# Optimization experiments

Measured on AMD Instinct MI355X. Metric: run time of the kernel, lower is better.

The kernel has to match this reference:

```python
import jax, jax.numpy as jnp
import numpy as np

L, B, Q, M, D, H, DH, DI = 4, 2, 1024, 1024, 1024, 16, 64, 4096


def setup_inputs() -> dict:
    key = jax.random.key(0)
    ks = jax.random.split(key, 10)
    s = 0.02
    return {
        "x": jax.random.normal(ks[0], (B, Q, D), jnp.float32),
        "memory": jax.random.normal(ks[1], (L, B, M, D), jnp.float32),
        "W_qkv": jax.random.normal(ks[2], (L, D, 3 * H * DH), jnp.float32) * s,
        "W_r": jax.random.normal(ks[3], (D, H * DH), jnp.float32) * s,
        "W_o": jax.random.normal(ks[4], (L, H * DH, D), jnp.float32) * s,
        "r_w_bias": jax.random.normal(ks[5], (H, DH), jnp.float32) * s,
        "r_r_bias": jax.random.normal(ks[6], (H, DH), jnp.float32) * s,
        "ln1_g": jnp.ones((L, D), jnp.float32),
        "ln1_b": jnp.zeros((L, D), jnp.float32),
        "ln2_g": jnp.ones((L, D), jnp.float32),
        "ln2_b": jnp.zeros((L, D), jnp.float32),
        "W_ff1": jax.random.normal(ks[7], (L, D, DI), jnp.float32) * s,
        "b_ff1": jnp.zeros((L, DI), jnp.float32),
        "W_ff2": jax.random.normal(ks[8], (L, DI, D), jnp.float32) * s,
        "b_ff2": jnp.zeros((L, D), jnp.float32),
    }


def _layernorm(x, g, b, eps=1e-5):
    mu = x.mean(-1, keepdims=True)
    var = ((x - mu) ** 2).mean(-1, keepdims=True)
    return (x - mu) * jax.lax.rsqrt(var + eps) * g + b


def _rel_shift(x):
    # Transformer-XL relative shift trick; x: [B, H, Q, K]
    b, h, q, k = x.shape
    x = jnp.pad(x, ((0, 0), (0, 0), (0, 0), (1, 0)))
    return x.reshape(b, h, k + 1, q)[:, :, 1:, :].reshape(b, h, q, k)


def reference(x, memory, W_qkv, W_r, W_o, r_w_bias, r_r_bias,
              ln1_g, ln1_b, ln2_g, ln2_b, W_ff1, b_ff1, W_ff2, b_ff2):
    Bsz, qlen, d = x.shape
    mlen = memory.shape[2]
    klen = mlen + qlen
    # sinusoidal relative position embedding for positions klen-1 .. 0
    pos = jnp.arange(klen - 1, -1, -1, dtype=x.dtype)
    inv_freq = 1.0 / (10000.0 ** (jnp.arange(0, d, 2, dtype=x.dtype) / d))
    sinusoid = pos[:, None] * inv_freq[None, :]
    p = jnp.concatenate([jnp.sin(sinusoid), jnp.cos(sinusoid)], axis=-1)  # [K, D]
    # causal mask with memory: query i may attend key j iff j <= i + mlen
    qi = jnp.arange(qlen)[:, None]
    kj = jnp.arange(klen)[None, :]
    blocked = kj > (qi + mlen)  # [Q, K]
    scale = 1.0 / np.sqrt(DH).astype(np.float32)
    for l in range(L):
        x_mem = jnp.concatenate([memory[l], x], axis=1)  # [B, K, D]
        heads = x_mem @ W_qkv[l]  # [B, K, 3*H*DH]
        qh, kh, vh = jnp.split(heads, 3, axis=-1)
        qh = qh[:, mlen:].reshape(Bsz, qlen, H, DH)
        kh = kh.reshape(Bsz, klen, H, DH)
        vh = vh.reshape(Bsz, klen, H, DH)
        r = (p @ W_r).reshape(klen, H, DH)  # [K, H, DH]
        AC = jnp.einsum('bqhd,bkhd->bhqk', qh + r_w_bias, kh)
        BD = _rel_shift(jnp.einsum('bqhd,khd->bhqk', qh + r_r_bias, r))
        score = (AC + BD) * scale
        score = jnp.where(blocked[None, None], -1e30, score)
        attn = jax.nn.softmax(score, axis=-1)
        out = jnp.einsum('bhqk,bkhd->bqhd', attn, vh).reshape(Bsz, qlen, H * DH) @ W_o[l]
        x = _layernorm(x + out, ln1_g[l], ln1_b[l])
        ff = jax.nn.relu(x @ W_ff1[l] + b_ff1[l]) @ W_ff2[l] + b_ff2[l]
        x = _layernorm(x + ff, ln2_g[l], ln2_b[l])
    return x
```

## Files before the change

kernel.cpp:

```cpp
#include <hip/hip_runtime.h>
#include <math.h>

#define L_  4
#define B_  2
#define Q_  1024
#define M_  1024
#define D_  1024
#define H_  16
#define DH_ 64
#define DI_ 4096
#define KL_ (M_ + Q_)

typedef __attribute__((ext_vector_type(8))) short short8v;
typedef __attribute__((ext_vector_type(4))) float f32x4;

__device__ __forceinline__ short f2bf(float f) {
    union { float f; unsigned u; } x; x.f = f;
    return (short)((x.u + 0x7FFFu + ((x.u >> 16) & 1)) >> 16);
}
__device__ __forceinline__ unsigned pack2bf(float a, float b) {
    return (unsigned)(unsigned short)f2bf(a) | ((unsigned)(unsigned short)f2bf(b) << 16);
}
__device__ __forceinline__ float bf2f(unsigned short u) {
    union { unsigned u; float f; } x; x.u = (unsigned)u << 16; return x.f;
}
__device__ __forceinline__ unsigned cvtpk(float lo, float hi) {
    unsigned r;
    asm("v_cvt_pk_bf16_f32 %0, %1, %2" : "=v"(r) : "v"(lo), "v"(hi));
    return r;
}
__device__ __forceinline__ void gload_lds16(const short* g, short* l) {
    __builtin_amdgcn_global_load_lds((const __attribute__((address_space(1))) unsigned int*)(const void*)g,
                                     (__attribute__((address_space(3))) unsigned int*)(void*)l, 16, 0, 0);
}
__device__ __forceinline__ int swz(int row) {
    return ((row & 7) ^ ((row >> 3) & 7)) << 3;
}

__global__ __launch_bounds__(256) void pos_emb_bf(short* __restrict__ p) {
    int idx = blockIdx.x * 256 + threadIdx.x;
    int k = idx >> 10;
    int i = idx & (D_ - 1);
    float pos = (float)(KL_ - 1 - k);
    int j = (i < D_ / 2) ? i : (i - D_ / 2);
    float invf = powf(10000.0f, -((float)(2 * j) / (float)D_));
    float ang = pos * invf;
    p[idx] = f2bf((i < D_ / 2) ? sinf(ang) : cosf(ang));
}

__global__ __launch_bounds__(256) void concat_bf(short* __restrict__ xmemb,
                                                 const float* __restrict__ mem_l,
                                                 const float* __restrict__ xc) {
    int idx = blockIdx.x * 256 + threadIdx.x;
    int d = idx & (D_ - 1);
    int k = (idx >> 10) & (KL_ - 1);
    int b = idx >> 21;
    float v = (k < M_) ? mem_l[((size_t)(b * M_ + k)) * D_ + d]
                       : xc[((size_t)(b * Q_ + (k - M_))) * D_ + d];
    xmemb[idx] = f2bf(v);
}

__global__ __launch_bounds__(256) void transp_bf(const float* __restrict__ in,
                                                 short* __restrict__ out,
                                                 int K, int N) {
    __shared__ float t[32][33];
    int r = threadIdx.x >> 3, c4 = (threadIdx.x & 7) * 4;
    float4 v = *(const float4*)(in + (size_t)(blockIdx.y * 32 + r) * N + blockIdx.x * 32 + c4);
    t[r][c4 + 0] = v.x; t[r][c4 + 1] = v.y; t[r][c4 + 2] = v.z; t[r][c4 + 3] = v.w;
    __syncthreads();
    uint2 o;
    o.x = pack2bf(t[c4 + 0][r], t[c4 + 1][r]);
    o.y = pack2bf(t[c4 + 2][r], t[c4 + 3][r]);
    *(uint2*)(out + (size_t)(blockIdx.x * 32 + r) * K + blockIdx.y * 32 + c4) = o;
}

template <int BIAS, int RELU, int OMODE, int TN, int KS = 1>
__global__ __launch_bounds__(256, 2) void gemm_bf(const short* __restrict__ A,
                                                  const short* __restrict__ BT,
                                                  const float* __restrict__ bias,
                                                  float* __restrict__ Cf,
                                                  short* __restrict__ C0,
                                                  short* __restrict__ C1,
                                                  short* __restrict__ C2,
                                                  int M, int N, int K) {
    __shared__ short A_s[128 * 32];
    __shared__ short B_s[TN * 32];
    const int tid = threadIdx.x;
    const int lane = tid & 63, w = tid >> 6;
    const int l15 = lane & 15, l4 = lane >> 4;
    constexpr int MF = (TN == 128) ? 4 : 2;
    const int wr = (TN == 128) ? (w >> 1) : w;
    const int wc = (TN == 128) ? (w & 1) : 0;
    const int arow0 = 32 * ((TN == 128) ? 2 * wr : w);
    const int brow0 = (TN == 128) ? 64 * wc : 0;
    const int row0 = blockIdx.y * 128, col0 = blockIdx.x * TN;
    const int kz = (KS == 2) ? blockIdx.z : 0;
    const int Kh = (KS == 2) ? (K >> 1) : K;
    const int kb = kz * Kh;

    const int lrow = lane >> 2;
    const int lk = (lane & 3) * 8;
    const short* Ag = A + (size_t)(row0 + 32 * w) * K;
    const short* Bg = BT + (size_t)(col0 + ((TN == 128) ? 32 : 16) * w) * K;

    f32x4 acc[MF][4] = {};

    for (int k0 = kb; k0 < kb + Kh; k0 += 32) {
        __syncthreads();
        gload_lds16(Ag + (size_t)lrow * K + k0 + lk,        &A_s[(32 * w) * 32]);
        gload_lds16(Ag + (size_t)(16 + lrow) * K + k0 + lk, &A_s[(32 * w + 16) * 32]);
        if (TN == 128) {
            gload_lds16(Bg + (size_t)lrow * K + k0 + lk,        &B_s[(32 * w) * 32]);
            gload_lds16(Bg + (size_t)(16 + lrow) * K + k0 + lk, &B_s[(32 * w + 16) * 32]);
        } else {
            gload_lds16(Bg + (size_t)lrow * K + k0 + lk,        &B_s[(16 * w) * 32]);
        }
        __syncthreads();
        short8v a[MF], bfr[4];
#pragma unroll
        for (int m = 0; m < MF; m++) a[m] = *(const short8v*)&A_s[(arow0 + 16 * m + l15) * 32 + 8 * l4];
#pragma unroll
        for (int n = 0; n < 4; n++) bfr[n] = *(const short8v*)&B_s[(brow0 + 16 * n + l15) * 32 + 8 * l4];
#pragma unroll
        for (int m = 0; m < MF; m++)
#pragma unroll
            for (int n = 0; n < 4; n++)
                acc[m][n] = __builtin_amdgcn_mfma_f32_16x16x32_bf16(a[m], bfr[n], acc[m][n], 0, 0, 0);
    }

    float* Cfz = Cf + (size_t)kz * M * N;
#pragma unroll
    for (int n = 0; n < 4; n++) {
        int col = col0 + brow0 + 16 * n + l15;
        float bv = (BIAS && (KS == 1 || kz == 0)) ? bias[col] : 0.0f;
#pragma unroll
        for (int m = 0; m < MF; m++) {
#pragma unroll
            for (int r = 0; r < 4; r++) {
                int row = row0 + arow0 + 16 * m + 4 * l4 + r;
                float v = acc[m][n][r] + bv;
                if (RELU) v = fmaxf(v, 0.0f);
                if (OMODE == 0) {
                    Cfz[(size_t)row * N + col] = v;
                } else if (OMODE == 1) {
                    C0[(size_t)row * N + col] = f2bf(v);
                } else {
                    int part = col >> 10, cc = col & 1023;
                    short* dst = part == 0 ? C0 : (part == 1 ? C1 : C2);
                    dst[(size_t)row * 1024 + cc] = f2bf(v);
                }
            }
        }
    }
}

__global__ __launch_bounds__(256, 2) void attn_mfma(const short* __restrict__ qbf,
                                                    const short* __restrict__ kbf,
                                                    const short* __restrict__ vbf,
                                                    const short* __restrict__ rbh,
                                                    const float* __restrict__ rwb,
                                                    const float* __restrict__ rrb,
                                                    short* __restrict__ attnob) {
    __shared__ short K_s[2][64 * 64];
    __shared__ short V_T[2][64 * 64];
    __shared__ short R_s[256 * 64];
    __shared__ short P_s[4][16 * 64];

    const int tid = threadIdx.x;
    const int lane = tid & 63, w = tid >> 6;
    const int l15 = lane & 15, l4 = lane >> 4;
    const int lr8 = lane >> 3, oct = lane & 7;
    const int d0 = (tid & 7) * 8;

    const int wg = blockIdx.x;
    const int xcd = wg & 7;
    const int qp = (wg >> 3) & 15;
    const int bl = (wg >> 7) & 3;
    const int h = xcd * 2 + (bl & 1);
    const int b = bl >> 1;
    const int qi = (qp & 1) ? (15 - (qp >> 1)) : (qp >> 1);
    const int q0 = qi * 64;
    const int nt = qi + 17;
    const int jbase0 = (Q_ - 64) - q0;

    size_t qrow = ((size_t)(b * KL_ + M_ + q0 + 16 * w + l15)) * 1024 + h * 64;
    union U8 { uint4 u; unsigned short us[8]; };
    U8 qa, qb2;
    qa.u  = *(const uint4*)(qbf + qrow + 8 * l4);
    qb2.u = *(const uint4*)(qbf + qrow + 32 + 8 * l4);
    short8v qwf0, qwf1, qrf0, qrf1;
#pragma unroll
    for (int i = 0; i < 8; i++) {
        float qv0 = bf2f(qa.us[i]), qv1 = bf2f(qb2.us[i]);
        int c0 = h * 64 + 8 * l4 + i, c1 = c0 + 32;
        qwf0[i] = f2bf(qv0 + rwb[c0]); qwf1[i] = f2bf(qv1 + rwb[c1]);
        qrf0[i] = f2bf(qv0 + rrb[c0]); qrf1[i] = f2bf(qv1 + rrb[c1]);
    }

#pragma unroll
    for (int c = 0; c < 2; c++) {
        int R0 = 16 * w + 8 * c;
        int row = R0 + lr8;
        gload_lds16(kbf + ((size_t)(b * KL_) + row) * 1024 + h * 64 + ((oct * 8) ^ swz(row)),
                    &K_s[0][R0 * 64]);
        gload_lds16(kbf + ((size_t)(b * KL_) + 64 + row) * 1024 + h * 64 + ((oct * 8) ^ swz(row)),
                    &K_s[1][R0 * 64]);
    }
#pragma unroll
    for (int c = 0; c < 8; c++) {
        int R0 = 64 * w + 8 * c;
        int row = R0 + lr8;
        int jl = jbase0 + row;
        gload_lds16(rbh + (size_t)jl * 1024 + h * 64 + ((oct * 8) ^ swz(row)),
                    &R_s[R0 * 64]);
    }
    {
        U8 cv0[2];
#pragma unroll
        for (int it = 0; it < 2; it++) {
            int rr = (tid + it * 256) >> 3;
            cv0[it].u = *(const uint4*)(vbf + ((size_t)(b * KL_) + rr) * 1024 + h * 64 + d0);
        }
#pragma unroll
        for (int it = 0; it < 2; it++) {
            int rr = (tid + it * 256) >> 3;
#pragma unroll
            for (int i = 0; i < 8; i++)
                V_T[0][(d0 + i) * 64 + (rr ^ swz(d0 + i))] = (short)cv0[it].us[i];
        }
    }
    asm volatile("s_waitcnt vmcnt(0) lgkmcnt(0)" ::: "memory");
    __builtin_amdgcn_sched_barrier(0);
    __builtin_amdgcn_s_barrier();
    __builtin_amdgcn_sched_barrier(0);

    f32x4 o[4];
    float m_r[4], l_p[4];
#pragma unroll
    for (int j = 0; j < 4; j++) o[j] = (f32x4){0.f, 0.f, 0.f, 0.f};
#pragma unroll
    for (int r = 0; r < 4; r++) { m_r[r] = -1e30f; l_p[r] = 0.0f; }

    int sl[4];
#pragma unroll
    for (int r = 0; r < 4; r++)
        sl[r] = (lane & 48) | ((l15 + 15 - (4 * l4 + r)) & 15);

    short* P_w = &P_s[w][0];
    const int rbase = 16 * (3 - w);

    f32x4 acA[4], zfA[5], acB[4], zfB[5];
#pragma unroll
    for (int j = 0; j < 4; j++) {
        int kk = 16 * j + l15, sz = swz(kk);
        short8v b0 = *(const short8v*)&K_s[0][kk * 64 + ((8 * l4) ^ sz)];
        short8v b1 = *(const short8v*)&K_s[0][kk * 64 + ((32 + 8 * l4) ^ sz)];
        f32x4 z = {0.f, 0.f, 0.f, 0.f};
        z = __builtin_amdgcn_mfma_f32_16x16x32_bf16(qwf0, b0, z, 0, 0, 0);
        z = __builtin_amdgcn_mfma_f32_16x16x32_bf16(qwf1, b1, z, 0, 0, 0);
        acA[j] = z;
    }
#pragma unroll
    for (int jb = 0; jb < 5; jb++) {
        int rp = (rbase + 16 * jb + l15) & 255;
        int sz = swz(rp);
        short8v b0 = *(const short8v*)&R_s[rp * 64 + ((8 * l4) ^ sz)];
        short8v b1 = *(const short8v*)&R_s[rp * 64 + ((32 + 8 * l4) ^ sz)];
        f32x4 z = {0.f, 0.f, 0.f, 0.f};
        z = __builtin_amdgcn_mfma_f32_16x16x32_bf16(qrf0, b0, z, 0, 0, 0);
        z = __builtin_amdgcn_mfma_f32_16x16x32_bf16(qrf1, b1, z, 0, 0, 0);
        zfA[jb] = z;
    }

    auto body = [&](f32x4 (&ac)[4], f32x4 (&zf)[5], f32x4 (&acn)[4], f32x4 (&zfn)[5], int t)
        __attribute__((always_inline)) {
        const int cb = t & 1, nb = (t + 1) & 1;
        uint4 pv2[2];
        if (t + 1 < nt) {
#pragma unroll
            for (int it = 0; it < 2; it++) {
                int rr = (tid + it * 256) >> 3;
                pv2[it] = *(const uint4*)(vbf + ((size_t)(b * KL_) + 64 * (t + 1) + rr) * 1024 + h * 64 + d0);
            }
        }
        if (t + 2 < nt) {
#pragma unroll
            for (int c = 0; c < 2; c++) {
                int R0 = 16 * w + 8 * c;
                int row = R0 + lr8;
                gload_lds16(kbf + ((size_t)(b * KL_) + 64 * (t + 2) + row) * 1024 + h * 64 + ((oct * 8) ^ swz(row)),
                            &K_s[cb][R0 * 64]);
            }
#pragma unroll
            for (int c = 0; c < 2; c++) {
                int R0 = 16 * w + 8 * c;
                int l0 = 64 * t + 256 + R0 + lr8;
                int ph = l0 & 255;
                int jl = jbase0 + l0;
                if (jl > KL_ - 1) jl = KL_ - 1;
                gload_lds16(rbh + (size_t)jl * 1024 + h * 64 + ((oct * 8) ^ swz(ph)),
                            &R_s[((64 * t + 256 + R0) & 255) * 64]);
            }
        }
        __builtin_amdgcn_sched_barrier(0);

        if (t + 1 < nt) {
            __builtin_amdgcn_s_setprio(1);
#pragma unroll
            for (int j = 0; j < 4; j++) {
                int kk = 16 * j + l15, sz = swz(kk);
                short8v b0 = *(const short8v*)&K_s[nb][kk * 64 + ((8 * l4) ^ sz)];
                short8v b1 = *(const short8v*)&K_s[nb][kk * 64 + ((32 + 8 * l4) ^ sz)];
                f32x4 z = {0.f, 0.f, 0.f, 0.f};
                z = __builtin_amdgcn_mfma_f32_16x16x32_bf16(qwf0, b0, z, 0, 0, 0);
                z = __builtin_amdgcn_mfma_f32_16x16x32_bf16(qwf1, b1, z, 0, 0, 0);
                acn[j] = z;
            }
#pragma unroll
            for (int jb = 0; jb < 5; jb++) {
                int rp = (64 * (t + 1) + rbase + 16 * jb + l15) & 255;
                int sz = swz(rp);
                short8v b0 = *(const short8v*)&R_s[rp * 64 + ((8 * l4) ^ sz)];
                short8v b1 = *(const short8v*)&R_s[rp * 64 + ((32 + 8 * l4) ^ sz)];
                f32x4 z = {0.f, 0.f, 0.f, 0.f};
                z = __builtin_amdgcn_mfma_f32_16x16x32_bf16(qrf0, b0, z, 0, 0, 0);
                z = __builtin_amdgcn_mfma_f32_16x16x32_bf16(qrf1, b1, z, 0, 0, 0);
                zfn[jb] = z;
            }
            __builtin_amdgcn_s_setprio(0);
        }

        float sv[4][4], lmax[4];
#pragma unroll
        for (int r = 0; r < 4; r++) {
            int row = 4 * l4 + r;
            float bq[5];
#pragma unroll
            for (int s = 0; s < 5; s++) bq[s] = __shfl(zf[s][r], sl[r]);
#pragma unroll
            for (int j = 0; j < 4; j++) {
                float bd = (l15 > row) ? bq[j + 1] : bq[j];
                sv[j][r] = (ac[j][r] + bd) * 0.125f;
            }
        }
        if (t == nt - 1) {
#pragma unroll
            for (int j = 0; j < 4; j++)
#pragma unroll
                for (int r = 0; r < 4; r++)
                    if (64 * t + 16 * j + l15 > q0 + 16 * w + 4 * l4 + r + M_) sv[j][r] = -1e30f;
        }
#pragma unroll
        for (int r = 0; r < 4; r++) lmax[r] = fmaxf(fmaxf(sv[0][r], sv[1][r]), fmaxf(sv[2][r], sv[3][r]));
        bool ok = true;
#pragma unroll
        for (int r = 0; r < 4; r++) ok = ok && (lmax[r] <= m_r[r] + 8.0f);
        if (!__all(ok)) {
#pragma unroll
            for (int r = 0; r < 4; r++) {
                float v = lmax[r];
                v = fmaxf(v, __shfl_xor(v, 1));
                v = fmaxf(v, __shfl_xor(v, 2));
                v = fmaxf(v, __shfl_xor(v, 4));
                v = fmaxf(v, __shfl_xor(v, 8));
                float mnew = fmaxf(m_r[r], v);
                float c = __expf(m_r[r] - mnew);
                m_r[r] = mnew;
                l_p[r] *= c;
#pragma unroll
                for (int jd = 0; jd < 4; jd++) o[jd][r] *= c;
            }
        }
#pragma unroll
        for (int j = 0; j < 4; j++)
#pragma unroll
            for (int r = 0; r < 4; r++) {
                float pp = __expf(sv[j][r] - m_r[r]);
                sv[j][r] = pp;
                l_p[r] += pp;
            }

#pragma unroll
        for (int r = 0; r < 4; r++) {
            int row = 4 * l4 + r;
            int sz = swz(row);
#pragma unroll
            for (int j = 0; j < 4; j += 2) {
                unsigned pk = cvtpk(sv[j][r], sv[j + 1][r]);
                P_w[row * 64 + ((16 * j + l15) ^ sz)] = (short)(pk & 0xffffu);
                P_w[row * 64 + ((16 * (j + 1) + l15) ^ sz)] = (short)(pk >> 16);
            }
        }
        int szp = swz(l15);
        short8v pa0 = *(const short8v*)&P_w[l15 * 64 + ((8 * l4) ^ szp)];
        short8v pa1 = *(const short8v*)&P_w[l15 * 64 + ((32 + 8 * l4) ^ szp)];
        __builtin_amdgcn_s_setprio(1);
#pragma unroll
        for (int jd = 0; jd < 4; jd++) {
            int dd = 16 * jd + l15, sz = swz(dd);
            short8v v0 = *(const short8v*)&V_T[cb][dd * 64 + ((8 * l4) ^ sz)];
            short8v v1 = *(const short8v*)&V_T[cb][dd * 64 + ((32 + 8 * l4) ^ sz)];
            o[jd] = __builtin_amdgcn_mfma_f32_16x16x32_bf16(pa0, v0, o[jd], 0, 0, 0);
            o[jd] = __builtin_amdgcn_mfma_f32_16x16x32_bf16(pa1, v1, o[jd], 0, 0, 0);
        }
        __builtin_amdgcn_s_setprio(0);

        if (t + 1 < nt) {
#pragma unroll
            for (int it = 0; it < 2; it++) {
                int rr = (tid + it * 256) >> 3;
                U8 cv; cv.u = pv2[it];
#pragma unroll
                for (int i = 0; i < 8; i++)
                    V_T[nb][(d0 + i) * 64 + (rr ^ swz(d0 + i))] = (short)cv.us[i];
            }
            asm volatile("s_waitcnt vmcnt(0) lgkmcnt(0)" ::: "memory");
            __builtin_amdgcn_sched_barrier(0);
            __builtin_amdgcn_s_barrier();
            __builtin_amdgcn_sched_barrier(0);
        }
    };

    int t = 0;
    while (t < nt) {
        body(acA, zfA, acB, zfB, t); t++;
        if (t >= nt) break;
        body(acB, zfB, acA, zfA, t); t++;
    }

    float l_r[4];
#pragma unroll
    for (int r = 0; r < 4; r++) {
        float v = l_p[r];
        v += __shfl_xor(v, 1);
        v += __shfl_xor(v, 2);
        v += __shfl_xor(v, 4);
        v += __shfl_xor(v, 8);
        l_r[r] = v;
    }
#pragma unroll
    for (int jd = 0; jd < 4; jd++) {
#pragma unroll
        for (int r = 0; r < 4; r++) {
            int qg = q0 + 16 * w + 4 * l4 + r;
            int dv = 16 * jd + l15;
            attnob[((size_t)(b * Q_ + qg)) * (H_ * DH_) + h * 64 + dv] = f2bf(o[jd][r] / l_r[r]);
        }
    }
}

__global__ __launch_bounds__(256) void ln_kernel(float* __restrict__ x,
                                                 short* __restrict__ xb,
                                                 const float* __restrict__ a1,
                                                 const float* __restrict__ a2,
                                                 const float* __restrict__ g,
                                                 const float* __restrict__ bb) {
    __shared__ float red[8];
    int row = blockIdx.x;
    int tid = threadIdx.x;
    float4 xv = ((const float4*)(x + (size_t)row * D_))[tid];
    float4 v1 = ((const float4*)(a1 + (size_t)row * D_))[tid];
    float4 v2 = ((const float4*)(a2 + (size_t)row * D_))[tid];
    float4 v;
    v.x = xv.x + v1.x + v2.x; v.y = xv.y + v1.y + v2.y;
    v.z = xv.z + v1.z + v2.z; v.w = xv.w + v1.w + v2.w;
    float s = v.x + v.y + v.z + v.w;
#pragma unroll
    for (int off = 32; off; off >>= 1) s += __shfl_xor(s, off);
    if ((tid & 63) == 0) red[tid >> 6] = s;
    __syncthreads();
    float mu = (red[0] + red[1] + red[2] + red[3]) * (1.0f / D_);
    float e0 = v.x - mu, e1 = v.y - mu, e2 = v.z - mu, e3 = v.w - mu;
    float sq = e0 * e0 + e1 * e1 + e2 * e2 + e3 * e3;
#pragma unroll
    for (int off = 32; off; off >>= 1) sq += __shfl_xor(sq, off);
    if ((tid & 63) == 0) red[4 + (tid >> 6)] = sq;
    __syncthreads();
    float var = (red[4] + red[5] + red[6] + red[7]) * (1.0f / D_);
    float rs = rsqrtf(var + 1e-5f);
    float4 gv = ((const float4*)g)[tid];
    float4 bv = ((const float4*)bb)[tid];
    float4 ov;
    ov.x = e0 * rs * gv.x + bv.x; ov.y = e1 * rs * gv.y + bv.y;
    ov.z = e2 * rs * gv.z + bv.z; ov.w = e3 * rs * gv.w + bv.w;
    ((float4*)(x + (size_t)row * D_))[tid] = ov;
    uint2 ob;
    ob.x = pack2bf(ov.x, ov.y);
    ob.y = pack2bf(ov.z, ov.w);
    *(uint2*)(xb + (size_t)row * D_ + tid * 4) = ob;
}

extern "C" void kernel_launch(void* const* d_in, const int* in_sizes, int n_in,
                              void* d_out, int out_size, void* d_ws, size_t ws_size,
                              hipStream_t stream) {
    const float* x    = (const float*)d_in[0];
    const float* mem  = (const float*)d_in[1];
    const float* Wqkv = (const float*)d_in[2];
    const float* Wr   = (const float*)d_in[3];
    const float* Wo   = (const float*)d_in[4];
    const float* rwb  = (const float*)d_in[5];
    const float* rrb  = (const float*)d_in[6];
    const float* ln1g = (const float*)d_in[7];
    const float* ln1b = (const float*)d_in[8];
    const float* ln2g = (const float*)d_in[9];
    const float* ln2b = (const float*)d_in[10];
    const float* Wff1 = (const float*)d_in[11];
    const float* bff1 = (const float*)d_in[12];
    const float* Wff2 = (const float*)d_in[13];
    const float* bff2 = (const float*)d_in[14];

    float* xc = (float*)d_out;

    short* WqkvT = (short*)d_ws;
    short* WoT   = WqkvT + 3145728;
    short* Wff1T = WoT + 1048576;
    short* Wff2T = Wff1T + 4194304;
    short* WrT   = Wff2T + 4194304;
    short* rbh   = WrT + 1048576;
    short* xmemb = rbh + 2097152;
    short* qbf   = xmemb + 4194304;
    short* kbf   = qbf + 4194304;
    short* vbf   = kbf + 4194304;
    short* attnob= vbf + 4194304;
    short* xcb   = attnob + 2097152;
    short* ff1ob = xcb + 2097152;
    float* addbuf= (float*)(ff1ob + 8388608);
    short* pbf   = ff1ob;

    transp_bf<<<dim3(32, 32), 256, 0, stream>>>(Wr, WrT, 1024, 1024);
    pos_emb_bf<<<(KL_ * D_) / 256, 256, 0, stream>>>(pbf);
    gemm_bf<0, 0, 1, 64><<<dim3(16, 16), 256, 0, stream>>>(
        pbf, WrT, nullptr, nullptr, rbh, nullptr, nullptr, KL_, 1024, 1024);

    hipMemcpyAsync(xc, x, (size_t)B_ * Q_ * D_ * sizeof(float),
                   hipMemcpyDeviceToDevice, stream);

    for (int l = 0; l < L_; l++) {
        const float* mem_l = mem + (size_t)l * B_ * M_ * D_;

        transp_bf<<<dim3(96, 32), 256, 0, stream>>>(Wqkv + (size_t)l * 3145728, WqkvT, 1024, 3072);
        transp_bf<<<dim3(32, 32), 256, 0, stream>>>(Wo + (size_t)l * 1048576, WoT, 1024, 1024);
        transp_bf<<<dim3(128, 32), 256, 0, stream>>>(Wff1 + (size_t)l * 4194304, Wff1T, 1024, 4096);
        transp_bf<<<dim3(32, 128), 256, 0, stream>>>(Wff2 + (size_t)l * 4194304, Wff2T, 4096, 1024);

        concat_bf<<<(B_ * KL_ * D_) / 256, 256, 0, stream>>>(xmemb, mem_l, xc);

        gemm_bf<0, 0, 2, 128><<<dim3(24, 32), 256, 0, stream>>>(
            xmemb, WqkvT, nullptr, nullptr, qbf, kbf, vbf, B_ * KL_, 3072, 1024);

        attn_mfma<<<B_ * H_ * (Q_ / 64), 256, 0, stream>>>(
            qbf, kbf, vbf, rbh, rwb, rrb, attnob);

        gemm_bf<0, 0, 0, 64, 2><<<dim3(16, 16, 2), 256, 0, stream>>>(
            attnob, WoT, nullptr, addbuf, nullptr, nullptr, nullptr, B_ * Q_, 1024, 1024);

        ln_kernel<<<B_ * Q_, 256, 0, stream>>>(xc, xcb, addbuf, addbuf + 2097152,
                                               ln1g + l * D_, ln1b + l * D_);

        gemm_bf<1, 1, 1, 128><<<dim3(32, 16), 256, 0, stream>>>(
            xcb, Wff1T, bff1 + (size_t)l * DI_, nullptr, ff1ob, nullptr, nullptr, B_ * Q_, 4096, 1024);

        gemm_bf<1, 0, 0, 64, 2><<<dim3(16, 16, 2), 256, 0, stream>>>(
            ff1ob, Wff2T, bff2 + (size_t)l * D_, addbuf, nullptr, nullptr, nullptr, B_ * Q_, 1024, 4096);

        ln_kernel<<<B_ * Q_, 256, 0, stream>>>(xc, xcb, addbuf, addbuf + 2097152,
                                               ln2g + l * D_, ln2b + l * D_);
    }
}
```

Measured before the change: 993.0 us.

## Compute Q only for current tokens and vectorize P stores via K-permuted V layout

Measured after the change: 1.049 ms. 1.06x slower.

```diff
diff --git a/kernel.cpp b/kernel.cpp
--- a/kernel.cpp
+++ b/kernel.cpp
@@ -36,6 +36,9 @@
 __device__ __forceinline__ int swz(int row) {
     return ((row & 7) ^ ((row >> 3) & 7)) << 3;
 }
+__device__ __forceinline__ int kperm(int k) {
+    return 4 * (k & 15) + (k >> 4);
+}
 
 __global__ __launch_bounds__(256) void pos_emb_bf(short* __restrict__ p) {
     int idx = blockIdx.x * 256 + threadIdx.x;
@@ -46,6 +49,14 @@
     float invf = powf(10000.0f, -((float)(2 * j) / (float)D_));
     float ang = pos * invf;
     p[idx] = f2bf((i < D_ / 2) ? sinf(ang) : cosf(ang));
+}
+
+__global__ __launch_bounds__(256) void bfconv_kernel(const float* __restrict__ in,
+                                                     short* __restrict__ out) {
+    int i = (blockIdx.x * 256 + threadIdx.x) * 4;
+    float4 v = *(const float4*)(in + i);
+    uint2 o; o.x = pack2bf(v.x, v.y); o.y = pack2bf(v.z, v.w);
+    *(uint2*)(out + i) = o;
 }
 
 __global__ __launch_bounds__(256) void concat_bf(short* __restrict__ xmemb,
@@ -183,7 +194,7 @@
     const int nt = qi + 17;
     const int jbase0 = (Q_ - 64) - q0;
 
-    size_t qrow = ((size_t)(b * KL_ + M_ + q0 + 16 * w + l15)) * 1024 + h * 64;
+    size_t qrow = ((size_t)(b * Q_ + q0 + 16 * w + l15)) * 1024 + h * 64;
     union U8 { uint4 u; unsigned short us[8]; };
     U8 qa, qb2;
     qa.u  = *(const uint4*)(qbf + qrow + 8 * l4);
@@ -224,9 +235,10 @@
 #pragma unroll
         for (int it = 0; it < 2; it++) {
             int rr = (tid + it * 256) >> 3;
+            int kp = kperm(rr);
 #pragma unroll
             for (int i = 0; i < 8; i++)
-                V_T[0][(d0 + i) * 64 + (rr ^ swz(d0 + i))] = (short)cv0[it].us[i];
+                V_T[0][(d0 + i) * 64 + (kp ^ swz(d0 + i))] = (short)cv0[it].us[i];
         }
     }
     asm volatile("s_waitcnt vmcnt(0) lgkmcnt(0)" ::: "memory");
@@ -383,13 +395,10 @@
 #pragma unroll
         for (int r = 0; r < 4; r++) {
             int row = 4 * l4 + r;
-            int sz = swz(row);
-#pragma unroll
-            for (int j = 0; j < 4; j += 2) {
-                unsigned pk = cvtpk(sv[j][r], sv[j + 1][r]);
-                P_w[row * 64 + ((16 * j + l15) ^ sz)] = (short)(pk & 0xffffu);
-                P_w[row * 64 + ((16 * (j + 1) + l15) ^ sz)] = (short)(pk >> 16);
-            }
+            uint2 pv;
+            pv.x = cvtpk(sv[0][r], sv[1][r]);
+            pv.y = cvtpk(sv[2][r], sv[3][r]);
+            *(uint2*)&P_w[row * 64 + ((4 * l15) ^ swz(row))] = pv;
         }
         int szp = swz(l15);
         short8v pa0 = *(const short8v*)&P_w[l15 * 64 + ((8 * l4) ^ szp)];
@@ -409,10 +418,11 @@
 #pragma unroll
             for (int it = 0; it < 2; it++) {
                 int rr = (tid + it * 256) >> 3;
+                int kp = kperm(rr);
                 U8 cv; cv.u = pv2[it];
 #pragma unroll
                 for (int i = 0; i < 8; i++)
-                    V_T[nb][(d0 + i) * 64 + (rr ^ swz(d0 + i))] = (short)cv.us[i];
+                    V_T[nb][(d0 + i) * 64 + (kp ^ swz(d0 + i))] = (short)cv.us[i];
             }
             asm volatile("s_waitcnt vmcnt(0) lgkmcnt(0)" ::: "memory");
             __builtin_amdgcn_sched_barrier(0);
@@ -534,6 +544,7 @@
 
     hipMemcpyAsync(xc, x, (size_t)B_ * Q_ * D_ * sizeof(float),
                    hipMemcpyDeviceToDevice, stream);
+    bfconv_kernel<<<(B_ * Q_ * D_) / 1024, 256, 0, stream>>>(xc, xcb);
 
     for (int l = 0; l < L_; l++) {
         const float* mem_l = mem + (size_t)l * B_ * M_ * D_;
@@ -545,8 +556,11 @@
 
         concat_bf<<<(B_ * KL_ * D_) / 256, 256, 0, stream>>>(xmemb, mem_l, xc);
 
-        gemm_bf<0, 0, 2, 128><<<dim3(24, 32), 256, 0, stream>>>(
-            xmemb, WqkvT, nullptr, nullptr, qbf, kbf, vbf, B_ * KL_, 3072, 1024);
+        gemm_bf<0, 0, 2, 128><<<dim3(16, 32), 256, 0, stream>>>(
+            xmemb, WqkvT + (size_t)1024 * 1024, nullptr, nullptr, kbf, vbf, nullptr,
+            B_ * KL_, 2048, 1024);
+        gemm_bf<0, 0, 1, 128><<<dim3(8, 16), 256, 0, stream>>>(
+            xcb, WqkvT, nullptr, nullptr, qbf, nullptr, nullptr, B_ * Q_, 1024, 1024);
 
         attn_mfma<<<B_ * H_ * (Q_ / 64), 256, 0, stream>>>(
             qbf, kbf, vbf, rbh, rwb, rrb, attnob);
```
